# Kernel tuning notes

Measured on AMD Instinct MI355X. Metric: run time of the kernel, lower is better.

## Reference

```python
import jax, jax.numpy as jnp
import numpy as np

N_NODES = 50000
N_EDGES = 800000
NUM_L0 = 3
H_CHANNELS = 32
NODE_INV_DIM = NUM_L0 * H_CHANNELS  # 96
H_DIM = 128  # edge_channels_list[0]
IN_DIM = H_DIM + 2 * NODE_INV_DIM  # 320
LN_EPS = 1e-5


def setup_inputs() -> dict:
    key = jax.random.key(0)
    ks = jax.random.split(key, 8)
    node_invariant = jax.random.normal(ks[0], (N_NODES, NODE_INV_DIM), dtype=jnp.float32)
    edge_features = jax.random.normal(ks[1], (N_EDGES, H_DIM), dtype=jnp.float32)
    edge_index = jax.random.randint(ks[2], (2, N_EDGES), 0, N_NODES, dtype=jnp.int32)
    # MLP params (scaled like torch default init ~ 1/sqrt(fan_in))
    W1 = jax.random.normal(ks[3], (IN_DIM, H_DIM), dtype=jnp.float32) / np.sqrt(IN_DIM)
    b1 = jnp.zeros((H_DIM,), dtype=jnp.float32)
    W2 = jax.random.normal(ks[4], (H_DIM, H_DIM), dtype=jnp.float32) / np.sqrt(H_DIM)
    b2 = jnp.zeros((H_DIM,), dtype=jnp.float32)
    ln_gamma = jnp.ones((H_DIM,), dtype=jnp.float32)
    ln_beta = jnp.zeros((H_DIM,), dtype=jnp.float32)
    return {
        "node_invariant": node_invariant,
        "edge_features": edge_features,
        "edge_index": edge_index,
        "W1": W1, "b1": b1, "W2": W2, "b2": b2,
        "ln_gamma": ln_gamma, "ln_beta": ln_beta,
    }


def reference(node_invariant, edge_features, edge_index, W1, b1, W2, b2, ln_gamma, ln_beta):
    # expand_edge: gather per-edge source/destination node invariant (l=0) features
    src = node_invariant[edge_index[0]]   # [E, NODE_INV_DIM]
    dst = node_invariant[edge_index[1]]   # [E, NODE_INV_DIM]
    x = jnp.concatenate([src, dst, edge_features], axis=-1)  # [E, IN_DIM]
    # ff: Linear -> ReLU -> Linear
    h = jax.nn.relu(x @ W1 + b1) @ W2 + b2  # [E, H_DIM]
    # LayerNorm over last dim
    mu = jnp.mean(h, axis=-1, keepdims=True)
    var = jnp.mean(jnp.square(h - mu), axis=-1, keepdims=True)
    hn = (h - mu) * jax.lax.rsqrt(var + LN_EPS) * ln_gamma + ln_beta
    # residual edge update
    return edge_features + hn
```

## Files before the change

### kernel.cpp

```cpp
#include <hip/hip_runtime.h>
#include <stdint.h>

#define N_H    128
#define N_INV  96
#define HS     132
#define EPSF   134
#define TILES  2
#define NWAVE  8
#define CHUNK  256
#define NBLK   256
#define KS1    10
#define KS2    4
#define W1_BYTES 81920
#define W2_BYTES 32768
#define W_BYTES  (W1_BYTES + W2_BYTES)
#define WBUF     4352
#define BIAS_OFF (W_BYTES + NWAVE * WBUF)
#define SMEM_BYTES (BIAS_OFF + 2048)

typedef __bf16 bf16x8 __attribute__((ext_vector_type(8)));
typedef float  f32x4  __attribute__((ext_vector_type(4)));

__device__ __forceinline__ unsigned short f2bf(float f) {
    union { float f; unsigned u; } v; v.f = f;
    unsigned u = v.u;
    u += 0x7FFFu + ((u >> 16) & 1u);
    return (unsigned short)(u >> 16);
}

__global__ void prep_weights(const float* __restrict__ W1,
                             const float* __restrict__ W2,
                             unsigned short* __restrict__ w1p,
                             unsigned short* __restrict__ w2p) {
    int idx = blockIdx.x * blockDim.x + threadIdx.x;
    if (idx < KS1 * 8 * 64 * 8) {
        int j = idx & 7, lane = (idx >> 3) & 63, nt = (idx >> 9) & 7, ks = idx >> 12;
        int k = ks * 32 + (lane >> 4) * 8 + j;
        int n = nt * 16 + (lane & 15);
        w1p[idx] = f2bf(W1[(size_t)k * N_H + n]);
    } else {
        int r = idx - KS1 * 8 * 64 * 8;
        if (r < KS2 * 8 * 64 * 8) {
            int j = r & 7, lane = (r >> 3) & 63, nt = (r >> 9) & 7, ks = r >> 12;
            int k = ks * 32 + (lane >> 4) * 8 + j;
            int n = nt * 16 + (lane & 15);
            w2p[r] = f2bf(W2[(size_t)k * N_H + n]);
        }
    }
}

__global__ void prep_ninv(const float* __restrict__ ninv,
                          unsigned short* __restrict__ nb, int n4) {
    int i = blockIdx.x * blockDim.x + threadIdx.x;
    if (i < n4) {
        float4 v = ((const float4*)ninv)[i];
        ((ushort4*)nb)[i] = make_ushort4(f2bf(v.x), f2bf(v.y), f2bf(v.z), f2bf(v.w));
    }
}

__global__ __launch_bounds__(512, 2)
void edge_mlp(const unsigned short* __restrict__ ninvb, const float* __restrict__ ef,
              const int* __restrict__ ei,
              const unsigned short* __restrict__ wpk,
              const float* __restrict__ b1g, const float* __restrict__ b2g,
              const float* __restrict__ gg, const float* __restrict__ btg,
              float* __restrict__ out, int E, int cbase, int crem) {
    extern __shared__ __align__(16) char smem[];

    const int tid  = threadIdx.x;
    const int wv   = tid >> 6;
    const int lane = tid & 63;
    const int lr   = lane & 15;
    const int lkg  = lane >> 4;
    const int lk   = lkg * 8;
    const int qr   = lkg * 4;

    const int b     = blockIdx.x;
    const int c0    = b * cbase + (b < crem ? b : crem);
    const int cnt   = cbase + (b < crem ? 1 : 0);
    if (cnt <= 0) return;
    const int clast = c0 + cnt - 1;

    {
        const char* gsrc = (const char*)wpk;
        #pragma unroll
        for (int i = 0; i < 14; ++i) {
            int ch = wv * 14 + i;
            __builtin_amdgcn_global_load_lds(
                (const __attribute__((address_space(1))) void*)(gsrc + ch * 1024 + lane * 16),
                (__attribute__((address_space(3))) void*)(smem + ch * 1024),
                16, 0, 0);
        }
        if (wv == 0) {
            const float* srcs[4] = { b1g, b2g, gg, btg };
            #pragma unroll
            for (int a = 0; a < 4; ++a) {
                #pragma unroll
                for (int h = 0; h < 2; ++h) {
                    __builtin_amdgcn_global_load_lds(
                        (const __attribute__((address_space(1))) void*)(srcs[a] + h * 64 + lane),
                        (__attribute__((address_space(3))) void*)(smem + BIAS_OFF + a * 512 + h * 256),
                        4, 0, 0);
                }
            }
        }
    }

    const float* b1l = (const float*)(smem + BIAS_OFF);
    const float* b2l = (const float*)(smem + BIAS_OFF + 512);
    const float* gl  = (const float*)(smem + BIAS_OFF + 1024);
    const float* btl = (const float*)(smem + BIAS_OFF + 1536);

    bf16x8 an[TILES][6];
    f32x4  efa[TILES][4][2];
    int sA[TILES], dA[TILES], eS[TILES], eD[TILES];
    {
        #pragma unroll
        for (int t = 0; t < TILES; ++t) {
            int er = c0 * CHUNK + wv * 32 + t * 16 + lr;
            int ee = er < E ? er : E - 1;
            int s0 = ei[ee], d0 = ei[(size_t)E + ee];
            #pragma unroll
            for (int q = 0; q < 6; ++q) {
                int row = q < 3 ? s0 : d0;
                an[t][q] = *(const bf16x8*)(ninvb + (size_t)row * N_INV + (q % 3) * 32 + lk);
            }
            const float* ap = ef + (size_t)ee * N_H;
            #pragma unroll
            for (int j = 0; j < 4; ++j) {
                efa[t][j][0] = *(const f32x4*)(ap + j * 32 + lk);
                efa[t][j][1] = *(const f32x4*)(ap + j * 32 + lk + 4);
            }
        }
        int c1 = c0 + 1 <= clast ? c0 + 1 : clast;
        #pragma unroll
        for (int t = 0; t < TILES; ++t) {
            int er = c1 * CHUNK + wv * 32 + t * 16 + lr;
            int ee = er < E ? er : E - 1;
            sA[t] = ei[ee]; dA[t] = ei[(size_t)E + ee];
        }
        int c2 = c0 + 2 <= clast ? c0 + 2 : clast;
        #pragma unroll
        for (int t = 0; t < TILES; ++t) {
            int er = c2 * CHUNK + wv * 32 + t * 16 + lr;
            int ee = er < E ? er : E - 1;
            eS[t] = ei[ee]; eD[t] = ei[(size_t)E + ee];
        }
    }

    __syncthreads();

    char* buf = smem + W_BYTES + wv * WBUF;
    __bf16* hb = (__bf16*)buf;
    float* ep = (float*)buf;

    for (int c = c0; c <= clast; ++c) {
        f32x4 acc[TILES][8] = {};
        #pragma unroll
        for (int ks = 0; ks < KS1; ++ks) {
            bf16x8 bfr[8];
            #pragma unroll
            for (int nt = 0; nt < 8; ++nt)
                bfr[nt] = *(const bf16x8*)(smem + ((ks * 8 + nt) << 10) + (lane << 4));
            #pragma unroll
            for (int t = 0; t < TILES; ++t) {
                bf16x8 a;
                if (ks < 6) {
                    a = an[t][ks];
                } else {
                    const int j = ks - 6;
                    union { __bf16 e[8]; bf16x8 v; } ua;
                    #pragma unroll
                    for (int m = 0; m < 4; ++m) {
                        ua.e[m]     = (__bf16)efa[t][j][0][m];
                        ua.e[4 + m] = (__bf16)efa[t][j][1][m];
                    }
                    a = ua.v;
                }
                __builtin_amdgcn_s_setprio(1);
                #pragma unroll
                for (int nt = 0; nt < 8; ++nt)
                    acc[t][nt] = __builtin_amdgcn_mfma_f32_16x16x32_bf16(a, bfr[nt], acc[t][nt], 0, 0, 0);
                __builtin_amdgcn_s_setprio(0);
            }
        }

        const int eb = c * CHUNK + wv * 32;

        #pragma unroll
        for (int t = 0; t < TILES; ++t) {
            #pragma unroll
            for (int nt = 0; nt < 8; ++nt) {
                float bb = b1l[nt * 16 + lr];
                #pragma unroll
                for (int i = 0; i < 4; ++i) {
                    float v = acc[t][nt][i] + bb;
                    v = v > 0.0f ? v : 0.0f;
                    hb[(qr + i) * HS + nt * 16 + lr] = (__bf16)v;
                }
            }
            __builtin_amdgcn_wave_barrier();

            f32x4 res[2][4];
            #pragma unroll
            for (int h = 0; h < 2; ++h) {
                #pragma unroll
                for (int it = 0; it < 4; ++it) {
                    int cid = it * 64 + lane;
                    int row = cid >> 5, c4 = (cid & 31) << 2;
                    int erow = eb + t * 16 + 8 * h + row;
                    int ec = erow < E ? erow : E - 1;
                    res[h][it] = *(const f32x4*)(ef + (size_t)ec * N_H + c4);
                }
            }

            f32x4 acc2[8] = {};
            #pragma unroll
            for (int ks = 0; ks < KS2; ++ks) {
                bf16x8 a = *(const bf16x8*)((const char*)hb + lr * (HS * 2) + ks * 64 + lkg * 16);
                __builtin_amdgcn_s_setprio(1);
                #pragma unroll
                for (int nt = 0; nt < 8; ++nt) {
                    bf16x8 w = *(const bf16x8*)(smem + W1_BYTES + ((ks * 8 + nt) << 10) + (lane << 4));
                    acc2[nt] = __builtin_amdgcn_mfma_f32_16x16x32_bf16(a, w, acc2[nt], 0, 0, 0);
                }
                __builtin_amdgcn_s_setprio(0);
            }

            if (t == 0) {
                #pragma unroll
                for (int tt = 0; tt < TILES; ++tt) {
                    #pragma unroll
                    for (int q = 0; q < 6; ++q) {
                        int row = q < 3 ? sA[tt] : dA[tt];
                        an[tt][q] = *(const bf16x8*)(ninvb + (size_t)row * N_INV + (q % 3) * 32 + lk);
                    }
                }
                sA[0] = eS[0]; sA[1] = eS[1]; dA[0] = eD[0]; dA[1] = eD[1];
                int c3 = c + 3 <= clast ? c + 3 : clast;
                #pragma unroll
                for (int tt = 0; tt < TILES; ++tt) {
                    int er = c3 * CHUNK + wv * 32 + tt * 16 + lr;
                    int ee = er < E ? er : E - 1;
                    eS[tt] = ei[ee]; eD[tt] = ei[(size_t)E + ee];
                }
            }

            float vals[8][4];
            float s1[4] = {0.f, 0.f, 0.f, 0.f};
            float s2[4] = {0.f, 0.f, 0.f, 0.f};
            #pragma unroll
            for (int nt = 0; nt < 8; ++nt) {
                float bb = b2l[nt * 16 + lr];
                #pragma unroll
                for (int i = 0; i < 4; ++i) {
                    float v = acc2[nt][i] + bb;
                    vals[nt][i] = v;
                    s1[i] += v;
                    s2[i] += v * v;
                }
            }
            #pragma unroll
            for (int m = 1; m < 16; m <<= 1) {
                #pragma unroll
                for (int i = 0; i < 4; ++i) {
                    s1[i] += __shfl_xor(s1[i], m);
                    s2[i] += __shfl_xor(s2[i], m);
                }
            }
            float mu[4], rs[4];
            #pragma unroll
            for (int i = 0; i < 4; ++i) {
                mu[i] = s1[i] * (1.0f / 128.0f);
                float var = s2[i] * (1.0f / 128.0f) - mu[i] * mu[i];
                rs[i] = rsqrtf(var + 1e-5f);
            }

            #pragma unroll
            for (int h = 0; h < 2; ++h) {
                if ((lkg >> 1) == h) {
                    #pragma unroll
                    for (int nt = 0; nt < 8; ++nt) {
                        int cc = nt * 16 + lr;
                        float g  = gl[cc];
                        float bt = btl[cc];
                        #pragma unroll
                        for (int i = 0; i < 4; ++i)
                            ep[(qr - 8 * h + i) * EPSF + cc] = (vals[nt][i] - mu[i]) * rs[i] * g + bt;
                    }
                }
                __builtin_amdgcn_wave_barrier();
                #pragma unroll
                for (int it = 0; it < 4; ++it) {
                    int cid = it * 64 + lane;
                    int row = cid >> 5, c4 = (cid & 31) << 2;
                    int erow = eb + t * 16 + 8 * h + row;
                    if (erow < E) {
                        f32x4 nv = *(const f32x4*)(ep + row * EPSF + c4);
                        *(f32x4*)(out + (size_t)erow * N_H + c4) = nv + res[h][it];
                    }
                }
                __builtin_amdgcn_wave_barrier();
            }
        }

        {
            int cn = c + 1 <= clast ? c + 1 : clast;
            #pragma unroll
            for (int t = 0; t < TILES; ++t) {
                int er = cn * CHUNK + wv * 32 + t * 16 + lr;
                int ee = er < E ? er : E - 1;
                const float* ap = ef + (size_t)ee * N_H;
                #pragma unroll
                for (int j = 0; j < 4; ++j) {
                    efa[t][j][0] = *(const f32x4*)(ap + j * 32 + lk);
                    efa[t][j][1] = *(const f32x4*)(ap + j * 32 + lk + 4);
                }
            }
        }
    }
}

extern "C" void kernel_launch(void* const* d_in, const int* in_sizes, int n_in,
                              void* d_out, int out_size, void* d_ws, size_t ws_size,
                              hipStream_t stream) {
    const float* ninv = (const float*)d_in[0];
    const float* ef   = (const float*)d_in[1];
    const int*   ei   = (const int*)d_in[2];
    const float* W1   = (const float*)d_in[3];
    const float* b1   = (const float*)d_in[4];
    const float* W2   = (const float*)d_in[5];
    const float* b2   = (const float*)d_in[6];
    const float* g    = (const float*)d_in[7];
    const float* bt   = (const float*)d_in[8];
    float* out = (float*)d_out;

    const int E = in_sizes[1] / N_H;
    const int NNODE = in_sizes[0] / N_INV;

    unsigned short* w1p = (unsigned short*)d_ws;
    unsigned short* w2p = w1p + KS1 * 8 * 64 * 8;
    unsigned short* nb  = w2p + KS2 * 8 * 64 * 8;

    hipFuncSetAttribute((const void*)edge_mlp,
                        hipFuncAttributeMaxDynamicSharedMemorySize, SMEM_BYTES);

    int prep_total = (KS1 + KS2) * 8 * 64 * 8;
    prep_weights<<<(prep_total + 255) / 256, 256, 0, stream>>>(W1, W2, w1p, w2p);

    int n4 = NNODE * N_INV / 4;
    prep_ninv<<<(n4 + 255) / 256, 256, 0, stream>>>(ninv, nb, n4);

    int nchunks = (E + CHUNK - 1) / CHUNK;
    int cbase = nchunks / NBLK;
    int crem  = nchunks - cbase * NBLK;
    edge_mlp<<<NBLK, 512, SMEM_BYTES, stream>>>(nb, ef, ei, w1p, b1, b2, g, bt,
                                                out, E, cbase, crem);
}
```

Before: 263.6 us.

## Use 16 waves of one 16-row tile each with streamed second-layer staging

The block grows from 8 waves with two 16-edge tiles each to 16 waves with one tile each. The hidden activation is staged through a small per-wave 16x32 bf16 buffer, one K-slice at a time, interleaved with the second-layer MFMAs, which shrinks per-wave LDS. Residual loads are split around the second GEMM, and node-feature prefetch now follows the first GEMM. The intent is to raise wave-level parallelism and latency hiding at the cost of more waves competing for LDS weights and lower per-wave instruction-level parallelism. The __launch_bounds__(1024, 4) hint cannot be met given the LDS footprint.

```diff
diff --git a/kernel.cpp b/kernel.cpp
--- a/kernel.cpp
+++ b/kernel.cpp
@@ -3,10 +3,9 @@
 
 #define N_H    128
 #define N_INV  96
-#define HS     132
 #define EPSF   134
-#define TILES  2
-#define NWAVE  8
+#define HPS    36
+#define NWAVE  16
 #define CHUNK  256
 #define NBLK   256
 #define KS1    10
@@ -14,11 +13,12 @@
 #define W1_BYTES 81920
 #define W2_BYTES 32768
 #define W_BYTES  (W1_BYTES + W2_BYTES)
-#define WBUF     4352
+#define WBUF     2176
 #define BIAS_OFF (W_BYTES + NWAVE * WBUF)
 #define SMEM_BYTES (BIAS_OFF + 2048)
 
 typedef __bf16 bf16x8 __attribute__((ext_vector_type(8)));
+typedef __bf16 bf16x4 __attribute__((ext_vector_type(4)));
 typedef float  f32x4  __attribute__((ext_vector_type(4)));
 
 __device__ __forceinline__ unsigned short f2bf(float f) {
@@ -58,7 +58,7 @@
     }
 }
 
-__global__ __launch_bounds__(512, 2)
+__global__ __launch_bounds__(1024, 4)
 void edge_mlp(const unsigned short* __restrict__ ninvb, const float* __restrict__ ef,
               const int* __restrict__ ei,
               const unsigned short* __restrict__ wpk,
@@ -84,8 +84,8 @@
     {
         const char* gsrc = (const char*)wpk;
         #pragma unroll
-        for (int i = 0; i < 14; ++i) {
-            int ch = wv * 14 + i;
+        for (int i = 0; i < 7; ++i) {
+            int ch = wv * 7 + i;
             __builtin_amdgcn_global_load_lds(
                 (const __attribute__((address_space(1))) void*)(gsrc + ch * 1024 + lane * 16),
                 (__attribute__((address_space(3))) void*)(smem + ch * 1024),
@@ -111,211 +111,197 @@
     const float* gl  = (const float*)(smem + BIAS_OFF + 1024);
     const float* btl = (const float*)(smem + BIAS_OFF + 1536);
 
-    bf16x8 an[TILES][6];
-    f32x4  efa[TILES][4][2];
-    int sA[TILES], dA[TILES], eS[TILES], eD[TILES];
+    bf16x8 an[6];
+    f32x4  efa[4][2];
+    int sA, dA, eS, eD;
     {
-        #pragma unroll
-        for (int t = 0; t < TILES; ++t) {
-            int er = c0 * CHUNK + wv * 32 + t * 16 + lr;
-            int ee = er < E ? er : E - 1;
-            int s0 = ei[ee], d0 = ei[(size_t)E + ee];
-            #pragma unroll
-            for (int q = 0; q < 6; ++q) {
-                int row = q < 3 ? s0 : d0;
-                an[t][q] = *(const bf16x8*)(ninvb + (size_t)row * N_INV + (q % 3) * 32 + lk);
-            }
-            const float* ap = ef + (size_t)ee * N_H;
-            #pragma unroll
-            for (int j = 0; j < 4; ++j) {
-                efa[t][j][0] = *(const f32x4*)(ap + j * 32 + lk);
-                efa[t][j][1] = *(const f32x4*)(ap + j * 32 + lk + 4);
-            }
+        int er = c0 * CHUNK + wv * 16 + lr;
+        int ee = er < E ? er : E - 1;
+        int s0 = ei[ee], d0 = ei[(size_t)E + ee];
+        #pragma unroll
+        for (int q = 0; q < 6; ++q) {
+            int row = q < 3 ? s0 : d0;
+            an[q] = *(const bf16x8*)(ninvb + (size_t)row * N_INV + (q % 3) * 32 + lk);
+        }
+        const float* ap = ef + (size_t)ee * N_H;
+        #pragma unroll
+        for (int j = 0; j < 4; ++j) {
+            efa[j][0] = *(const f32x4*)(ap + j * 32 + lk);
+            efa[j][1] = *(const f32x4*)(ap + j * 32 + lk + 4);
         }
         int c1 = c0 + 1 <= clast ? c0 + 1 : clast;
-        #pragma unroll
-        for (int t = 0; t < TILES; ++t) {
-            int er = c1 * CHUNK + wv * 32 + t * 16 + lr;
-            int ee = er < E ? er : E - 1;
-            sA[t] = ei[ee]; dA[t] = ei[(size_t)E + ee];
-        }
+        int e1 = c1 * CHUNK + wv * 16 + lr; e1 = e1 < E ? e1 : E - 1;
+        sA = ei[e1]; dA = ei[(size_t)E + e1];
         int c2 = c0 + 2 <= clast ? c0 + 2 : clast;
-        #pragma unroll
-        for (int t = 0; t < TILES; ++t) {
-            int er = c2 * CHUNK + wv * 32 + t * 16 + lr;
-            int ee = er < E ? er : E - 1;
-            eS[t] = ei[ee]; eD[t] = ei[(size_t)E + ee];
-        }
+        int e2 = c2 * CHUNK + wv * 16 + lr; e2 = e2 < E ? e2 : E - 1;
+        eS = ei[e2]; eD = ei[(size_t)E + e2];
     }
 
     __syncthreads();
 
     char* buf = smem + W_BYTES + wv * WBUF;
-    __bf16* hb = (__bf16*)buf;
-    float* ep = (float*)buf;
+    __bf16* hp = (__bf16*)buf;
+    float*  ep = (float*)buf;
 
     for (int c = c0; c <= clast; ++c) {
-        f32x4 acc[TILES][8] = {};
+        const int eb = c * CHUNK + wv * 16;
+
+        bf16x8 anef[4];
+        #pragma unroll
+        for (int j = 0; j < 4; ++j) {
+            union { __bf16 e[8]; bf16x8 v; } ua;
+            #pragma unroll
+            for (int m = 0; m < 4; ++m) {
+                ua.e[m]     = (__bf16)efa[j][0][m];
+                ua.e[4 + m] = (__bf16)efa[j][1][m];
+            }
+            anef[j] = ua.v;
+        }
+
+        f32x4 acc[8] = {};
         #pragma unroll
         for (int ks = 0; ks < KS1; ++ks) {
             bf16x8 bfr[8];
             #pragma unroll
             for (int nt = 0; nt < 8; ++nt)
                 bfr[nt] = *(const bf16x8*)(smem + ((ks * 8 + nt) << 10) + (lane << 4));
-            #pragma unroll
-            for (int t = 0; t < TILES; ++t) {
-                bf16x8 a;
-                if (ks < 6) {
-                    a = an[t][ks];
-                } else {
-                    const int j = ks - 6;
-                    union { __bf16 e[8]; bf16x8 v; } ua;
-                    #pragma unroll
-                    for (int m = 0; m < 4; ++m) {
-                        ua.e[m]     = (__bf16)efa[t][j][0][m];
-                        ua.e[4 + m] = (__bf16)efa[t][j][1][m];
-                    }
-                    a = ua.v;
-                }
-                __builtin_amdgcn_s_setprio(1);
-                #pragma unroll
-                for (int nt = 0; nt < 8; ++nt)
-                    acc[t][nt] = __builtin_amdgcn_mfma_f32_16x16x32_bf16(a, bfr[nt], acc[t][nt], 0, 0, 0);
-                __builtin_amdgcn_s_setprio(0);
-            }
-        }
-
-        const int eb = c * CHUNK + wv * 32;
-
-        #pragma unroll
-        for (int t = 0; t < TILES; ++t) {
-            #pragma unroll
-            for (int nt = 0; nt < 8; ++nt) {
+            bf16x8 a = (ks < 6) ? an[ks] : anef[ks - 6];
+            __builtin_amdgcn_s_setprio(1);
+            #pragma unroll
+            for (int nt = 0; nt < 8; ++nt)
+                acc[nt] = __builtin_amdgcn_mfma_f32_16x16x32_bf16(a, bfr[nt], acc[nt], 0, 0, 0);
+            __builtin_amdgcn_s_setprio(0);
+        }
+
+        #pragma unroll
+        for (int q = 0; q < 6; ++q) {
+            int row = q < 3 ? sA : dA;
+            an[q] = *(const bf16x8*)(ninvb + (size_t)row * N_INV + (q % 3) * 32 + lk);
+        }
+        sA = eS; dA = eD;
+        {
+            int c3 = c + 3 <= clast ? c + 3 : clast;
+            int e3 = c3 * CHUNK + wv * 16 + lr; e3 = e3 < E ? e3 : E - 1;
+            eS = ei[e3]; eD = ei[(size_t)E + e3];
+        }
+
+        f32x4 res[4][2];
+        #pragma unroll
+        for (int q = 0; q < 2; ++q) {
+            #pragma unroll
+            for (int it = 0; it < 2; ++it) {
+                int row4 = (it << 1) + (lane >> 5);
+                int c4   = (lane & 31) << 2;
+                int erow = eb + 4 * q + row4;
+                int ec   = erow < E ? erow : E - 1;
+                res[q][it] = *(const f32x4*)(ef + (size_t)ec * N_H + c4);
+            }
+        }
+
+        f32x4 acc2[8] = {};
+        #pragma unroll
+        for (int ks = 0; ks < KS2; ++ks) {
+            #pragma unroll
+            for (int p = 0; p < 2; ++p) {
+                int nt = 2 * ks + p;
                 float bb = b1l[nt * 16 + lr];
                 #pragma unroll
                 for (int i = 0; i < 4; ++i) {
-                    float v = acc[t][nt][i] + bb;
+                    float v = acc[nt][i] + bb;
                     v = v > 0.0f ? v : 0.0f;
-                    hb[(qr + i) * HS + nt * 16 + lr] = (__bf16)v;
+                    hp[(qr + i) * HPS + p * 16 + lr] = (__bf16)v;
                 }
             }
             __builtin_amdgcn_wave_barrier();
-
-            f32x4 res[2][4];
-            #pragma unroll
-            for (int h = 0; h < 2; ++h) {
-                #pragma unroll
-                for (int it = 0; it < 4; ++it) {
-                    int cid = it * 64 + lane;
-                    int row = cid >> 5, c4 = (cid & 31) << 2;
-                    int erow = eb + t * 16 + 8 * h + row;
-                    int ec = erow < E ? erow : E - 1;
-                    res[h][it] = *(const f32x4*)(ef + (size_t)ec * N_H + c4);
-                }
-            }
-
-            f32x4 acc2[8] = {};
-            #pragma unroll
-            for (int ks = 0; ks < KS2; ++ks) {
-                bf16x8 a = *(const bf16x8*)((const char*)hb + lr * (HS * 2) + ks * 64 + lkg * 16);
-                __builtin_amdgcn_s_setprio(1);
+            union { bf16x4 h[2]; bf16x8 v; } ua;
+            ua.h[0] = *(const bf16x4*)(hp + lr * HPS + lk);
+            ua.h[1] = *(const bf16x4*)(hp + lr * HPS + lk + 4);
+            __builtin_amdgcn_s_setprio(1);
+            #pragma unroll
+            for (int nt = 0; nt < 8; ++nt) {
+                bf16x8 w = *(const bf16x8*)(smem + W1_BYTES + ((ks * 8 + nt) << 10) + (lane << 4));
+                acc2[nt] = __builtin_amdgcn_mfma_f32_16x16x32_bf16(ua.v, w, acc2[nt], 0, 0, 0);
+            }
+            __builtin_amdgcn_s_setprio(0);
+            __builtin_amdgcn_wave_barrier();
+        }
+
+        #pragma unroll
+        for (int q = 2; q < 4; ++q) {
+            #pragma unroll
+            for (int it = 0; it < 2; ++it) {
+                int row4 = (it << 1) + (lane >> 5);
+                int c4   = (lane & 31) << 2;
+                int erow = eb + 4 * q + row4;
+                int ec   = erow < E ? erow : E - 1;
+                res[q][it] = *(const f32x4*)(ef + (size_t)ec * N_H + c4);
+            }
+        }
+
+        float s1[4] = {0.f, 0.f, 0.f, 0.f};
+        float s2[4] = {0.f, 0.f, 0.f, 0.f};
+        #pragma unroll
+        for (int nt = 0; nt < 8; ++nt) {
+            float bb = b2l[nt * 16 + lr];
+            #pragma unroll
+            for (int i = 0; i < 4; ++i) {
+                float v = acc2[nt][i] + bb;
+                acc2[nt][i] = v;
+                s1[i] += v;
+                s2[i] += v * v;
+            }
+        }
+        #pragma unroll
+        for (int m = 1; m < 16; m <<= 1) {
+            #pragma unroll
+            for (int i = 0; i < 4; ++i) {
+                s1[i] += __shfl_xor(s1[i], m);
+                s2[i] += __shfl_xor(s2[i], m);
+            }
+        }
+        float mu[4], rs[4];
+        #pragma unroll
+        for (int i = 0; i < 4; ++i) {
+            mu[i] = s1[i] * (1.0f / 128.0f);
+            float var = s2[i] * (1.0f / 128.0f) - mu[i] * mu[i];
+            rs[i] = rsqrtf(var + 1e-5f);
+        }
+
+        #pragma unroll
+        for (int q = 0; q < 4; ++q) {
+            if (lkg == q) {
                 #pragma unroll
                 for (int nt = 0; nt < 8; ++nt) {
-                    bf16x8 w = *(const bf16x8*)(smem + W1_BYTES + ((ks * 8 + nt) << 10) + (lane << 4));
-                    acc2[nt] = __builtin_amdgcn_mfma_f32_16x16x32_bf16(a, w, acc2[nt], 0, 0, 0);
+                    int cc = nt * 16 + lr;
+                    float g  = gl[cc];
+                    float bt = btl[cc];
+                    #pragma unroll
+                    for (int i = 0; i < 4; ++i)
+                        ep[i * EPSF + cc] = (acc2[nt][i] - mu[i]) * rs[i] * g + bt;
                 }
-                __builtin_amdgcn_s_setprio(0);
-            }
-
-            if (t == 0) {
-                #pragma unroll
-                for (int tt = 0; tt < TILES; ++tt) {
-                    #pragma unroll
-                    for (int q = 0; q < 6; ++q) {
-                        int row = q < 3 ? sA[tt] : dA[tt];
-                        an[tt][q] = *(const bf16x8*)(ninvb + (size_t)row * N_INV + (q % 3) * 32 + lk);
-                    }
+            }
+            __builtin_amdgcn_wave_barrier();
+            #pragma unroll
+            for (int it = 0; it < 2; ++it) {
+                int row4 = (it << 1) + (lane >> 5);
+                int c4   = (lane & 31) << 2;
+                int erow = eb + 4 * q + row4;
+                if (erow < E) {
+                    f32x4 nv = *(const f32x4*)(ep + row4 * EPSF + c4);
+                    *(f32x4*)(out + (size_t)erow * N_H + c4) = nv + res[q][it];
                 }
-                sA[0] = eS[0]; sA[1] = eS[1]; dA[0] = eD[0]; dA[1] = eD[1];
-                int c3 = c + 3 <= clast ? c + 3 : clast;
-                #pragma unroll
-                for (int tt = 0; tt < TILES; ++tt) {
-                    int er = c3 * CHUNK + wv * 32 + tt * 16 + lr;
-                    int ee = er < E ? er : E - 1;
-                    eS[tt] = ei[ee]; eD[tt] = ei[(size_t)E + ee];
-                }
-            }
-
-            float vals[8][4];
-            float s1[4] = {0.f, 0.f, 0.f, 0.f};
-            float s2[4] = {0.f, 0.f, 0.f, 0.f};
-            #pragma unroll
-            for (int nt = 0; nt < 8; ++nt) {
-                float bb = b2l[nt * 16 + lr];
-                #pragma unroll
-                for (int i = 0; i < 4; ++i) {
-                    float v = acc2[nt][i] + bb;
-                    vals[nt][i] = v;
-                    s1[i] += v;
-                    s2[i] += v * v;
-                }
-            }
-            #pragma unroll
-            for (int m = 1; m < 16; m <<= 1) {
-                #pragma unroll
-                for (int i = 0; i < 4; ++i) {
-                    s1[i] += __shfl_xor(s1[i], m);
-                    s2[i] += __shfl_xor(s2[i], m);
-                }
-            }
-            float mu[4], rs[4];
-            #pragma unroll
-            for (int i = 0; i < 4; ++i) {
-                mu[i] = s1[i] * (1.0f / 128.0f);
-                float var = s2[i] * (1.0f / 128.0f) - mu[i] * mu[i];
-                rs[i] = rsqrtf(var + 1e-5f);
-            }
-
-            #pragma unroll
-            for (int h = 0; h < 2; ++h) {
-                if ((lkg >> 1) == h) {
-                    #pragma unroll
-                    for (int nt = 0; nt < 8; ++nt) {
-                        int cc = nt * 16 + lr;
-                        float g  = gl[cc];
-                        float bt = btl[cc];
-                        #pragma unroll
-                        for (int i = 0; i < 4; ++i)
-                            ep[(qr - 8 * h + i) * EPSF + cc] = (vals[nt][i] - mu[i]) * rs[i] * g + bt;
-                    }
-                }
-                __builtin_amdgcn_wave_barrier();
-                #pragma unroll
-                for (int it = 0; it < 4; ++it) {
-                    int cid = it * 64 + lane;
-                    int row = cid >> 5, c4 = (cid & 31) << 2;
-                    int erow = eb + t * 16 + 8 * h + row;
-                    if (erow < E) {
-                        f32x4 nv = *(const f32x4*)(ep + row * EPSF + c4);
-                        *(f32x4*)(out + (size_t)erow * N_H + c4) = nv + res[h][it];
-                    }
-                }
-                __builtin_amdgcn_wave_barrier();
-            }
+            }
+            __builtin_amdgcn_wave_barrier();
         }
 
         {
             int cn = c + 1 <= clast ? c + 1 : clast;
-            #pragma unroll
-            for (int t = 0; t < TILES; ++t) {
-                int er = cn * CHUNK + wv * 32 + t * 16 + lr;
-                int ee = er < E ? er : E - 1;
-                const float* ap = ef + (size_t)ee * N_H;
-                #pragma unroll
-                for (int j = 0; j < 4; ++j) {
-                    efa[t][j][0] = *(const f32x4*)(ap + j * 32 + lk);
-                    efa[t][j][1] = *(const f32x4*)(ap + j * 32 + lk + 4);
-                }
+            int en = cn * CHUNK + wv * 16 + lr; en = en < E ? en : E - 1;
+            const float* ap = ef + (size_t)en * N_H;
+            #pragma unroll
+            for (int j = 0; j < 4; ++j) {
+                efa[j][0] = *(const f32x4*)(ap + j * 32 + lk);
+                efa[j][1] = *(const f32x4*)(ap + j * 32 + lk + 4);
             }
         }
     }
@@ -354,6 +340,6 @@
     int nchunks = (E + CHUNK - 1) / CHUNK;
     int cbase = nchunks / NBLK;
     int crem  = nchunks - cbase * NBLK;
-    edge_mlp<<<NBLK, 512, SMEM_BYTES, stream>>>(nb, ef, ei, w1p, b1, b2, g, bt,
-                                                out, E, cbase, crem);
-}
+    edge_mlp<<<NBLK, 1024, SMEM_BYTES, stream>>>(nb, ef, ei, w1p, b1, b2, g, bt,
+                                                 out, E, cbase, crem);
+}
```

Result: slower. 408.5 us (+55.0%).

## Replace static per-block chunk split with per-wave atomic work stealing

Applied to the files above, without the earlier changes.

Each wave now pulls its own 32-edge work items from a global atomic counter, reset by a memset before launch, instead of each block owning a fixed contiguous range of 256-edge chunks. The aim is to balance load across waves and blocks and cut tail imbalance from the static split. The cost is an atomic per work item plus a memset launch. It also drops the separate vals array and reuses the acc2 registers, which may ease register pressure.

```diff
diff --git a/kernel.cpp b/kernel.cpp
--- a/kernel.cpp
+++ b/kernel.cpp
@@ -6,8 +6,6 @@
 #define HS     132
 #define EPSF   134
 #define TILES  2
-#define NWAVE  8
-#define CHUNK  256
 #define NBLK   256
 #define KS1    10
 #define KS2    4
@@ -15,6 +13,7 @@
 #define W2_BYTES 32768
 #define W_BYTES  (W1_BYTES + W2_BYTES)
 #define WBUF     4352
+#define NWAVE  8
 #define BIAS_OFF (W_BYTES + NWAVE * WBUF)
 #define SMEM_BYTES (BIAS_OFF + 2048)
 
@@ -64,7 +63,7 @@
               const unsigned short* __restrict__ wpk,
               const float* __restrict__ b1g, const float* __restrict__ b2g,
               const float* __restrict__ gg, const float* __restrict__ btg,
-              float* __restrict__ out, int E, int cbase, int crem) {
+              float* __restrict__ out, int E, unsigned* __restrict__ cnt) {
     extern __shared__ __align__(16) char smem[];
 
     const int tid  = threadIdx.x;
@@ -75,12 +74,6 @@
     const int lk   = lkg * 8;
     const int qr   = lkg * 4;
 
-    const int b     = blockIdx.x;
-    const int c0    = b * cbase + (b < crem ? b : crem);
-    const int cnt   = cbase + (b < crem ? 1 : 0);
-    if (cnt <= 0) return;
-    const int clast = c0 + cnt - 1;
-
     {
         const char* gsrc = (const char*)wpk;
         #pragma unroll
@@ -111,13 +104,21 @@
     const float* gl  = (const float*)(smem + BIAS_OFF + 1024);
     const float* btl = (const float*)(smem + BIAS_OFF + 1536);
 
+    int w0, w1, w2, w3;
+    {
+        int v = 0;
+        if (lane == 0) v = (int)atomicAdd(cnt, 3u);
+        v = __shfl(v, 0);
+        w0 = v; w1 = v + 1; w2 = v + 2;
+    }
+
     bf16x8 an[TILES][6];
     f32x4  efa[TILES][4][2];
     int sA[TILES], dA[TILES], eS[TILES], eD[TILES];
     {
         #pragma unroll
         for (int t = 0; t < TILES; ++t) {
-            int er = c0 * CHUNK + wv * 32 + t * 16 + lr;
+            int er = w0 * 32 + t * 16 + lr;
             int ee = er < E ? er : E - 1;
             int s0 = ei[ee], d0 = ei[(size_t)E + ee];
             #pragma unroll
@@ -132,17 +133,15 @@
                 efa[t][j][1] = *(const f32x4*)(ap + j * 32 + lk + 4);
             }
         }
-        int c1 = c0 + 1 <= clast ? c0 + 1 : clast;
         #pragma unroll
         for (int t = 0; t < TILES; ++t) {
-            int er = c1 * CHUNK + wv * 32 + t * 16 + lr;
+            int er = w1 * 32 + t * 16 + lr;
             int ee = er < E ? er : E - 1;
             sA[t] = ei[ee]; dA[t] = ei[(size_t)E + ee];
         }
-        int c2 = c0 + 2 <= clast ? c0 + 2 : clast;
         #pragma unroll
         for (int t = 0; t < TILES; ++t) {
-            int er = c2 * CHUNK + wv * 32 + t * 16 + lr;
+            int er = w2 * 32 + t * 16 + lr;
             int ee = er < E ? er : E - 1;
             eS[t] = ei[ee]; eD[t] = ei[(size_t)E + ee];
         }
@@ -154,7 +153,7 @@
     __bf16* hb = (__bf16*)buf;
     float* ep = (float*)buf;
 
-    for (int c = c0; c <= clast; ++c) {
+    while (w0 * 32 < E) {
         f32x4 acc[TILES][8] = {};
         #pragma unroll
         for (int ks = 0; ks < KS1; ++ks) {
@@ -185,7 +184,7 @@
             }
         }
 
-        const int eb = c * CHUNK + wv * 32;
+        const int eb = w0 * 32;
 
         #pragma unroll
         for (int t = 0; t < TILES; ++t) {
@@ -237,16 +236,19 @@
                     }
                 }
                 sA[0] = eS[0]; sA[1] = eS[1]; dA[0] = eD[0]; dA[1] = eD[1];
-                int c3 = c + 3 <= clast ? c + 3 : clast;
+                {
+                    int v = 0;
+                    if (lane == 0) v = (int)atomicAdd(cnt, 1u);
+                    w3 = __shfl(v, 0);
+                }
                 #pragma unroll
                 for (int tt = 0; tt < TILES; ++tt) {
-                    int er = c3 * CHUNK + wv * 32 + tt * 16 + lr;
+                    int er = w3 * 32 + tt * 16 + lr;
                     int ee = er < E ? er : E - 1;
                     eS[tt] = ei[ee]; eD[tt] = ei[(size_t)E + ee];
                 }
             }
 
-            float vals[8][4];
             float s1[4] = {0.f, 0.f, 0.f, 0.f};
             float s2[4] = {0.f, 0.f, 0.f, 0.f};
             #pragma unroll
@@ -255,7 +257,7 @@
                 #pragma unroll
                 for (int i = 0; i < 4; ++i) {
                     float v = acc2[nt][i] + bb;
-                    vals[nt][i] = v;
+                    acc2[nt][i] = v;
                     s1[i] += v;
                     s2[i] += v * v;
                 }
@@ -286,7 +288,7 @@
                         float bt = btl[cc];
                         #pragma unroll
                         for (int i = 0; i < 4; ++i)
-                            ep[(qr - 8 * h + i) * EPSF + cc] = (vals[nt][i] - mu[i]) * rs[i] * g + bt;
+                            ep[(qr - 8 * h + i) * EPSF + cc] = (acc2[nt][i] - mu[i]) * rs[i] * g + bt;
                     }
                 }
                 __builtin_amdgcn_wave_barrier();
@@ -305,10 +307,9 @@
         }
 
         {
-            int cn = c + 1 <= clast ? c + 1 : clast;
             #pragma unroll
             for (int t = 0; t < TILES; ++t) {
-                int er = cn * CHUNK + wv * 32 + t * 16 + lr;
+                int er = w1 * 32 + t * 16 + lr;
                 int ee = er < E ? er : E - 1;
                 const float* ap = ef + (size_t)ee * N_H;
                 #pragma unroll
@@ -318,6 +319,8 @@
                 }
             }
         }
+
+        w0 = w1; w1 = w2; w2 = w3;
     }
 }
 
@@ -341,6 +344,7 @@
     unsigned short* w1p = (unsigned short*)d_ws;
     unsigned short* w2p = w1p + KS1 * 8 * 64 * 8;
     unsigned short* nb  = w2p + KS2 * 8 * 64 * 8;
+    unsigned* cnt = (unsigned*)((char*)d_ws + 114688 + (size_t)NNODE * N_INV * 2);
 
     hipFuncSetAttribute((const void*)edge_mlp,
                         hipFuncAttributeMaxDynamicSharedMemorySize, SMEM_BYTES);
@@ -351,9 +355,8 @@
     int n4 = NNODE * N_INV / 4;
     prep_ninv<<<(n4 + 255) / 256, 256, 0, stream>>>(ninv, nb, n4);
 
-    int nchunks = (E + CHUNK - 1) / CHUNK;
-    int cbase = nchunks / NBLK;
-    int crem  = nchunks - cbase * NBLK;
+    hipMemsetAsync(cnt, 0, 4, stream);
+
     edge_mlp<<<NBLK, 512, SMEM_BYTES, stream>>>(nb, ef, ei, w1p, b1, b2, g, bt,
-                                                out, E, cbase, crem);
-}
+                                                out, E, cnt);
+}
```

New measurement: 368.5 us. 1.4x slower.
